# Performance work log

Hardware: AMD Instinct MI355X
Metric: run time of the kernel (lower is better)

The kernel has to match this reference:

```python
import jax, jax.numpy as jnp
import numpy as np

B, L, D, H = 2, 2048, 1024, 16
HD = D // H
SCALE = 1.0 / (HD ** 0.5)


def setup_inputs() -> dict:
    key = jax.random.key(0)
    ks = jax.random.split(key, 8)
    s = 0.02  # keep pre-softmax logits in a sane range
    return {
        "x": jax.random.normal(ks[0], (B, L, D), dtype=jnp.float32),
        "attn_biases": jax.random.normal(ks[1], (B, H, L, L), dtype=jnp.float32) * 0.1,
        "attn_mask": jnp.zeros((B, 1, L, L), dtype=jnp.float32),
        "Wq": jax.random.normal(ks[2], (D, D), dtype=jnp.float32) * s,
        "bq": jnp.zeros((D,), dtype=jnp.float32),
        "Wk": jax.random.normal(ks[3], (D, D), dtype=jnp.float32) * s,
        "bk": jnp.zeros((D,), dtype=jnp.float32),
        "Wv": jax.random.normal(ks[4], (D, D), dtype=jnp.float32) * s,
        "bv": jnp.zeros((D,), dtype=jnp.float32),
        "Wo": jax.random.normal(ks[5], (D, D), dtype=jnp.float32) * s,
        "bo": jnp.zeros((D,), dtype=jnp.float32),
    }


def reference(x, attn_biases, attn_mask, Wq, bq, Wk, bk, Wv, bv, Wo, bo):
    b, l, d = x.shape
    # torch nn.Linear: y = x @ W.T + b
    q = (x @ Wq.T + bq).reshape(b, l, H, HD)
    k = (x @ Wk.T + bk).reshape(b, l, H, HD)
    v = (x @ Wv.T + bv).reshape(b, l, H, HD)
    # scores: (B, H, Lq, Lk)
    scores = SCALE * jnp.einsum("bqhd,bkhd->bhqk", q, k)
    scores = scores + attn_biases + attn_mask
    probs = jax.nn.softmax(scores, axis=-1)
    out = jnp.einsum("bhqk,bkhd->bqhd", probs, v).reshape(b, l, d)
    return out @ Wo.T + bo
```

## Files before the change

### kernel.cpp

```cpp
#include <hip/hip_runtime.h>
#include <stdint.h>

#define SCALE_ 0.125f

typedef unsigned short u16;
typedef __attribute__((ext_vector_type(8))) __bf16 bf16x8;
typedef __attribute__((ext_vector_type(4))) float f32x4;
typedef __attribute__((ext_vector_type(4))) unsigned int u32x4;

__device__ __forceinline__ void gload16(const void* g, void* l) {
  __builtin_amdgcn_global_load_lds(
      (const __attribute__((address_space(1))) unsigned int*)g,
      (__attribute__((address_space(3))) unsigned int*)l, 16, 0, 0);
}

__device__ __forceinline__ u16 f2bf(float f) {
  union { float f; unsigned int u; } v; v.f = f;
  return (u16)((v.u + 0x7FFFu + ((v.u >> 16) & 1u)) >> 16);
}

__device__ __forceinline__ bf16x8 ld_bf8(const u16* p) {
  return *reinterpret_cast<const bf16x8*>(p);
}

__global__ __launch_bounds__(256) void cvt_kernel(
    const float* __restrict__ x, const float* __restrict__ wq,
    const float* __restrict__ wk, const float* __restrict__ wv,
    const float* __restrict__ wo, u16* __restrict__ ws) {
  long e0 = ((long)blockIdx.x * 256 + threadIdx.x) * 8;
  const float* src; u16* dst; long off;
  if (e0 < 4194304L) {
    src = x; dst = ws; off = e0;
  } else {
    long tt = e0 - 4194304L;
    int w = (int)(tt >> 20);
    off = tt & 1048575L;
    src = (w == 0) ? wq : (w == 1) ? wk : (w == 2) ? wv : wo;
    dst = ws + 4194304L + (long)w * 1048576L;
  }
  float4 f0 = *(const float4*)(src + off);
  float4 f1 = *(const float4*)(src + off + 4);
  union { u16 u[8]; u32x4 v; } r;
  r.u[0] = f2bf(f0.x); r.u[1] = f2bf(f0.y); r.u[2] = f2bf(f0.z); r.u[3] = f2bf(f0.w);
  r.u[4] = f2bf(f1.x); r.u[5] = f2bf(f1.y); r.u[6] = f2bf(f1.z); r.u[7] = f2bf(f1.w);
  *reinterpret_cast<u32x4*>(dst + off) = r.v;
}

__global__ __launch_bounds__(256) void gemm_bt(
    const u16* __restrict__ A,
    const u16* __restrict__ W0, const u16* __restrict__ W1, const u16* __restrict__ W2,
    const float* __restrict__ b0, const float* __restrict__ b1, const float* __restrict__ b2,
    void* __restrict__ d0, void* __restrict__ d1, void* __restrict__ d2,
    int mode_base) {
  __shared__ u16 lsA[128 * 32];
  __shared__ u16 lsB[128 * 32];

  const int z = blockIdx.z;
  const int mode = mode_base + z;
  const u16* W = (z == 0) ? W0 : (z == 1) ? W1 : W2;
  const float* bias = (z == 0) ? b0 : (z == 1) ? b1 : b2;
  void* dst = (z == 0) ? d0 : (z == 1) ? d1 : d2;
  const float scale = (mode == 0) ? SCALE_ : 1.0f;

  const int t = threadIdx.x;
  const int bm = blockIdx.y, bn = blockIdx.x;
  const int lane = t & 63, lr = lane & 15, lg = lane >> 4;
  const int wid = t >> 6, wr = wid >> 1, wc = wid & 1;

  f32x4 zero = {0.f, 0.f, 0.f, 0.f};
  f32x4 acc[4][4];
#pragma unroll
  for (int i = 0; i < 4; ++i)
#pragma unroll
    for (int j = 0; j < 4; ++j) acc[i][j] = zero;

  const u16* gA = A + (size_t)(bm * 128) * 1024;
  const u16* gB = W + (size_t)(bn * 128) * 1024;
  const int srow = t >> 2, scol = (t & 3) * 8;

  for (int kt = 0; kt < 32; ++kt) {
    const int k0 = kt * 32;
    __syncthreads();
    gload16(gA + (size_t)srow * 1024 + k0 + scol,        &lsA[t * 8]);
    gload16(gA + (size_t)(srow + 64) * 1024 + k0 + scol, &lsA[2048 + t * 8]);
    gload16(gB + (size_t)srow * 1024 + k0 + scol,        &lsB[t * 8]);
    gload16(gB + (size_t)(srow + 64) * 1024 + k0 + scol, &lsB[2048 + t * 8]);
    __syncthreads();

    bf16x8 af[4], bf[4];
#pragma unroll
    for (int mi = 0; mi < 4; ++mi)
      af[mi] = ld_bf8(&lsA[(wr * 64 + mi * 16 + lr) * 32 + lg * 8]);
#pragma unroll
    for (int ni = 0; ni < 4; ++ni)
      bf[ni] = ld_bf8(&lsB[(wc * 64 + ni * 16 + lr) * 32 + lg * 8]);
#pragma unroll
    for (int mi = 0; mi < 4; ++mi)
#pragma unroll
      for (int ni = 0; ni < 4; ++ni)
        acc[mi][ni] = __builtin_amdgcn_mfma_f32_16x16x32_bf16(af[mi], bf[ni], acc[mi][ni], 0, 0, 0);
  }

#pragma unroll
  for (int ni = 0; ni < 4; ++ni) {
    const int gcol = bn * 128 + wc * 64 + ni * 16 + lr;
    const float bv = bias[gcol];
#pragma unroll
    for (int mi = 0; mi < 4; ++mi) {
      const int growb = bm * 128 + wr * 64 + mi * 16 + lg * 4;
#pragma unroll
      for (int j = 0; j < 4; ++j) {
        const int grow = growb + j;
        const float val = (acc[mi][ni][j] + bv) * scale;
        if (mode == 3) {
          ((float*)dst)[(size_t)grow * 1024 + gcol] = val;
        } else {
          const int b = grow >> 11, l = grow & 2047, h = gcol >> 6, hd = gcol & 63;
          size_t idx;
          if (mode == 2) idx = (((size_t)(b * 16 + h)) * 64 + hd) * 2048 + l;
          else           idx = (((size_t)(b * 16 + h)) * 2048 + l) * 64 + hd;
          ((u16*)dst)[idx] = f2bf(val);
        }
      }
    }
  }
}

__global__ __launch_bounds__(256) void gemm_out64(
    const u16* __restrict__ A, const u16* __restrict__ W,
    const float* __restrict__ bias, float* __restrict__ out) {
  __shared__ u16 lsA[64 * 32];
  __shared__ u16 lsB[128 * 32];

  const int t = threadIdx.x;
  const int bm = blockIdx.y, bn = blockIdx.x;
  const int lane = t & 63, lr = lane & 15, lg = lane >> 4;
  const int wid = t >> 6;

  f32x4 zero = {0.f, 0.f, 0.f, 0.f};
  f32x4 acc[4][2];
#pragma unroll
  for (int i = 0; i < 4; ++i) { acc[i][0] = zero; acc[i][1] = zero; }

  const u16* gA = A + (size_t)(bm * 64) * 1024;
  const u16* gB = W + (size_t)(bn * 128) * 1024;
  const int srow = t >> 2, scol = (t & 3) * 8;

  for (int kt = 0; kt < 32; ++kt) {
    const int k0 = kt * 32;
    __syncthreads();
    gload16(gA + (size_t)srow * 1024 + k0 + scol,        &lsA[t * 8]);
    gload16(gB + (size_t)srow * 1024 + k0 + scol,        &lsB[t * 8]);
    gload16(gB + (size_t)(srow + 64) * 1024 + k0 + scol, &lsB[2048 + t * 8]);
    __syncthreads();

    bf16x8 af[4], bf[2];
#pragma unroll
    for (int mi = 0; mi < 4; ++mi)
      af[mi] = ld_bf8(&lsA[(mi * 16 + lr) * 32 + lg * 8]);
#pragma unroll
    for (int ni = 0; ni < 2; ++ni)
      bf[ni] = ld_bf8(&lsB[(wid * 32 + ni * 16 + lr) * 32 + lg * 8]);
#pragma unroll
    for (int mi = 0; mi < 4; ++mi)
#pragma unroll
      for (int ni = 0; ni < 2; ++ni)
        acc[mi][ni] = __builtin_amdgcn_mfma_f32_16x16x32_bf16(af[mi], bf[ni], acc[mi][ni], 0, 0, 0);
  }

#pragma unroll
  for (int ni = 0; ni < 2; ++ni) {
    const int gcol = bn * 128 + wid * 32 + ni * 16 + lr;
    const float bv = bias[gcol];
#pragma unroll
    for (int mi = 0; mi < 4; ++mi) {
      const int growb = bm * 64 + mi * 16 + lg * 4;
#pragma unroll
      for (int j = 0; j < 4; ++j)
        out[(size_t)(growb + j) * 1024 + gcol] = acc[mi][ni][j] + bv;
    }
  }
}

__global__ __launch_bounds__(256, 4) void attn_kernel(
    const u16* __restrict__ Q, const u16* __restrict__ Kb_, const u16* __restrict__ Vtb,
    const float* __restrict__ bias, const float* __restrict__ mask,
    u16* __restrict__ attn) {
  __shared__ u16 lsK[64 * 64];
  __shared__ u16 lsV[64 * 64];
  __shared__ u16 lsP[4][16 * 80];

  const int t = threadIdx.x, wid = t >> 6, lane = t & 63, lr = lane & 15, lg = lane >> 4;
  const int q0 = blockIdx.x * 64;
  const int h = blockIdx.y, b = blockIdx.z;
  const int bh = b * 16 + h;

  const u16* qb = Q + ((size_t)bh * 2048 + q0 + wid * 16) * 64;
  const u16* kb = Kb_ + (size_t)bh * 2048 * 64;
  const u16* vb = Vtb + (size_t)bh * 64 * 2048;
  const float* biasr = bias + (size_t)bh * 2048 * 2048;
  const float* maskr = mask + (size_t)b * 2048 * 2048;

  bf16x8 qf[2];
  qf[0] = ld_bf8(qb + (size_t)lr * 64 + lg * 8);
  qf[1] = ld_bf8(qb + (size_t)lr * 64 + 32 + lg * 8);

  float m[4] = {-1e30f, -1e30f, -1e30f, -1e30f};
  float lsum[4] = {0.f, 0.f, 0.f, 0.f};
  f32x4 zero = {0.f, 0.f, 0.f, 0.f};
  f32x4 o[4];
#pragma unroll
  for (int i = 0; i < 4; ++i) o[i] = zero;

  const int srow = t >> 3;
  const int swz = ((t & 7) ^ (srow & 7)) * 8;
  const int rsw = (lr & 7) * 8;
  const int qrow0 = q0 + wid * 16 + lg * 4;

  for (int kt = 0; kt < 32; ++kt) {
    const int k0 = kt * 64;

    float bb[4][4];
#pragma unroll
    for (int j = 0; j < 4; ++j) {
      const float* br = biasr + (size_t)(qrow0 + j) * 2048 + k0 + lr;
      const float* mr = maskr + (size_t)(qrow0 + j) * 2048 + k0 + lr;
#pragma unroll
      for (int n = 0; n < 4; ++n) bb[j][n] = br[n * 16] + mr[n * 16];
    }

    __syncthreads();
    gload16(kb + (size_t)(k0 + srow) * 64 + swz,        &lsK[t * 8]);
    gload16(kb + (size_t)(k0 + srow + 32) * 64 + swz,   &lsK[2048 + t * 8]);
    gload16(vb + (size_t)srow * 2048 + k0 + swz,        &lsV[t * 8]);
    gload16(vb + (size_t)(srow + 32) * 2048 + k0 + swz, &lsV[2048 + t * 8]);
    __syncthreads();

    f32x4 s[4];
#pragma unroll
    for (int n = 0; n < 4; ++n) s[n] = zero;
#pragma unroll
    for (int ks = 0; ks < 2; ++ks)
#pragma unroll
      for (int n = 0; n < 4; ++n) {
        bf16x8 kf = ld_bf8(&lsK[((n * 16 + lr) * 64 + ks * 32 + lg * 8) ^ rsw]);
        s[n] = __builtin_amdgcn_mfma_f32_16x16x32_bf16(qf[ks], kf, s[n], 0, 0, 0);
      }

#pragma unroll
    for (int j = 0; j < 4; ++j)
#pragma unroll
      for (int n = 0; n < 4; ++n) s[n][j] += bb[j][n];

    float corr[4];
#pragma unroll
    for (int i = 0; i < 4; ++i) {
      float mx = fmaxf(fmaxf(s[0][i], s[1][i]), fmaxf(s[2][i], s[3][i]));
      mx = fmaxf(mx, __shfl_xor(mx, 1));
      mx = fmaxf(mx, __shfl_xor(mx, 2));
      mx = fmaxf(mx, __shfl_xor(mx, 4));
      mx = fmaxf(mx, __shfl_xor(mx, 8));
      const float mnew = fmaxf(m[i], mx);
      const float c = __expf(m[i] - mnew);
      m[i] = mnew;
      float rs = 0.f;
#pragma unroll
      for (int n = 0; n < 4; ++n) {
        float p = __expf(s[n][i] - mnew);
        s[n][i] = p;
        rs += p;
      }
      rs += __shfl_xor(rs, 1); rs += __shfl_xor(rs, 2);
      rs += __shfl_xor(rs, 4); rs += __shfl_xor(rs, 8);
      lsum[i] = lsum[i] * c + rs;
      corr[i] = c;
    }
#pragma unroll
    for (int dt = 0; dt < 4; ++dt)
#pragma unroll
      for (int i = 0; i < 4; ++i) o[dt][i] *= corr[i];

#pragma unroll
    for (int n = 0; n < 4; ++n)
#pragma unroll
      for (int i = 0; i < 4; ++i)
        lsP[wid][(lg * 4 + i) * 80 + n * 16 + lr] = f2bf(s[n][i]);
    asm volatile("s_waitcnt lgkmcnt(0)" ::: "memory");
    __builtin_amdgcn_sched_barrier(0);

#pragma unroll
    for (int ks = 0; ks < 2; ++ks) {
      bf16x8 pa = ld_bf8(&lsP[wid][lr * 80 + ks * 32 + lg * 8]);
#pragma unroll
      for (int dt = 0; dt < 4; ++dt) {
        bf16x8 vf = ld_bf8(&lsV[((dt * 16 + lr) * 64 + ks * 32 + lg * 8) ^ rsw]);
        o[dt] = __builtin_amdgcn_mfma_f32_16x16x32_bf16(pa, vf, o[dt], 0, 0, 0);
      }
    }
  }

  float inv[4];
#pragma unroll
  for (int i = 0; i < 4; ++i) inv[i] = 1.0f / lsum[i];
#pragma unroll
  for (int dt = 0; dt < 4; ++dt) {
    const int dcol = h * 64 + dt * 16 + lr;
#pragma unroll
    for (int i = 0; i < 4; ++i)
      attn[((size_t)b * 2048 + qrow0 + i) * 1024 + dcol] = f2bf(o[dt][i] * inv[i]);
  }
}

extern "C" void kernel_launch(void* const* d_in, const int* in_sizes, int n_in,
                              void* d_out, int out_size, void* d_ws, size_t ws_size,
                              hipStream_t stream) {
  const float* x    = (const float*)d_in[0];
  const float* bias = (const float*)d_in[1];
  const float* mask = (const float*)d_in[2];
  const float* Wq   = (const float*)d_in[3];
  const float* bq   = (const float*)d_in[4];
  const float* Wk   = (const float*)d_in[5];
  const float* bk   = (const float*)d_in[6];
  const float* Wv   = (const float*)d_in[7];
  const float* bv   = (const float*)d_in[8];
  const float* Wo   = (const float*)d_in[9];
  const float* bo   = (const float*)d_in[10];
  float* out = (float*)d_out;

  u16* ws   = (u16*)d_ws;
  u16* xb   = ws;
  u16* wqb  = ws + 4194304L;
  u16* wkb  = wqb + 1048576L;
  u16* wvb  = wkb + 1048576L;
  u16* wob  = wvb + 1048576L;
  u16* Qb   = wob + 1048576L;
  u16* Kb   = Qb + 4194304L;
  u16* Vtb  = Kb + 4194304L;
  u16* attnb = Vtb + 4194304L;

  cvt_kernel<<<4096, 256, 0, stream>>>(x, Wq, Wk, Wv, Wo, ws);

  dim3 gqkv(8, 32, 3);
  gemm_bt<<<gqkv, 256, 0, stream>>>(xb, wqb, wkb, wvb, bq, bk, bv,
                                    (void*)Qb, (void*)Kb, (void*)Vtb, 0);

  attn_kernel<<<dim3(32, 16, 2), 256, 0, stream>>>(Qb, Kb, Vtb, bias, mask, attnb);

  gemm_out64<<<dim3(8, 64), 256, 0, stream>>>(attnb, wob, bo, out);
}
```

Before: 250.5 us.

## Prefetch next K/V tile and bias through registers to overlap with compute

Replaces the synchronous global_load_lds staging of K/V tiles with register prefetch: the next tile's K/V are loaded into registers at the start of each iteration and written to LDS after the PV MFMAs. Bias and mask loads for the next tile are also issued early, so their latency hides behind the softmax and matmul work. The trade-off is higher register pressure and an extra register-to-LDS write step, and the last iteration does one redundant reload.

```diff
diff --git a/kernel.cpp b/kernel.cpp
--- a/kernel.cpp
+++ b/kernel.cpp
@@ -212,29 +212,42 @@
 #pragma unroll
   for (int i = 0; i < 4; ++i) o[i] = zero;
 
-  const int srow = t >> 3;
-  const int swz = ((t & 7) ^ (srow & 7)) * 8;
+  const int srow = t >> 3, schunk = t & 7;
+  const int swc = (schunk ^ (srow & 7)) * 8;
+  const int gco = schunk * 8;
   const int rsw = (lr & 7) * 8;
   const int qrow0 = q0 + wid * 16 + lg * 4;
 
+  u16* wK0 = &lsK[srow * 64 + swc];
+  u16* wK1 = &lsK[(srow + 32) * 64 + swc];
+  u16* wV0 = &lsV[srow * 64 + swc];
+  u16* wV1 = &lsV[(srow + 32) * 64 + swc];
+
+  u32x4 rk0 = *(const u32x4*)(kb + (size_t)srow * 64 + gco);
+  u32x4 rk1 = *(const u32x4*)(kb + (size_t)(srow + 32) * 64 + gco);
+  u32x4 rv0 = *(const u32x4*)(vb + (size_t)srow * 2048 + gco);
+  u32x4 rv1 = *(const u32x4*)(vb + (size_t)(srow + 32) * 2048 + gco);
+  *(u32x4*)wK0 = rk0; *(u32x4*)wK1 = rk1;
+  *(u32x4*)wV0 = rv0; *(u32x4*)wV1 = rv1;
+  __syncthreads();
+
+  float bb[4][4];
+#pragma unroll
+  for (int j = 0; j < 4; ++j) {
+    const float* br = biasr + (size_t)(qrow0 + j) * 2048 + lr;
+    const float* mr = maskr + (size_t)(qrow0 + j) * 2048 + lr;
+#pragma unroll
+    for (int n = 0; n < 4; ++n) bb[j][n] = br[n * 16] + mr[n * 16];
+  }
+
   for (int kt = 0; kt < 32; ++kt) {
-    const int k0 = kt * 64;
-
-    float bb[4][4];
-#pragma unroll
-    for (int j = 0; j < 4; ++j) {
-      const float* br = biasr + (size_t)(qrow0 + j) * 2048 + k0 + lr;
-      const float* mr = maskr + (size_t)(qrow0 + j) * 2048 + k0 + lr;
-#pragma unroll
-      for (int n = 0; n < 4; ++n) bb[j][n] = br[n * 16] + mr[n * 16];
-    }
-
-    __syncthreads();
-    gload16(kb + (size_t)(k0 + srow) * 64 + swz,        &lsK[t * 8]);
-    gload16(kb + (size_t)(k0 + srow + 32) * 64 + swz,   &lsK[2048 + t * 8]);
-    gload16(vb + (size_t)srow * 2048 + k0 + swz,        &lsV[t * 8]);
-    gload16(vb + (size_t)(srow + 32) * 2048 + k0 + swz, &lsV[2048 + t * 8]);
-    __syncthreads();
+    const int ktn = (kt < 31) ? kt + 1 : 31;
+    const int k0n = ktn * 64;
+
+    rk0 = *(const u32x4*)(kb + (size_t)(k0n + srow) * 64 + gco);
+    rk1 = *(const u32x4*)(kb + (size_t)(k0n + srow + 32) * 64 + gco);
+    rv0 = *(const u32x4*)(vb + (size_t)srow * 2048 + k0n + gco);
+    rv1 = *(const u32x4*)(vb + (size_t)(srow + 32) * 2048 + k0n + gco);
 
     f32x4 s[4];
 #pragma unroll
@@ -252,7 +265,14 @@
 #pragma unroll
       for (int n = 0; n < 4; ++n) s[n][j] += bb[j][n];
 
-    float corr[4];
+#pragma unroll
+    for (int j = 0; j < 4; ++j) {
+      const float* br = biasr + (size_t)(qrow0 + j) * 2048 + k0n + lr;
+      const float* mr = maskr + (size_t)(qrow0 + j) * 2048 + k0n + lr;
+#pragma unroll
+      for (int n = 0; n < 4; ++n) bb[j][n] = br[n * 16] + mr[n * 16];
+    }
+
 #pragma unroll
     for (int i = 0; i < 4; ++i) {
       float mx = fmaxf(fmaxf(s[0][i], s[1][i]), fmaxf(s[2][i], s[3][i]));
@@ -273,12 +293,8 @@
       rs += __shfl_xor(rs, 1); rs += __shfl_xor(rs, 2);
       rs += __shfl_xor(rs, 4); rs += __shfl_xor(rs, 8);
       lsum[i] = lsum[i] * c + rs;
-      corr[i] = c;
-    }
-#pragma unroll
-    for (int dt = 0; dt < 4; ++dt)
-#pragma unroll
-      for (int i = 0; i < 4; ++i) o[dt][i] *= corr[i];
+      o[0][i] *= c; o[1][i] *= c; o[2][i] *= c; o[3][i] *= c;
+    }
 
 #pragma unroll
     for (int n = 0; n < 4; ++n)
@@ -297,6 +313,11 @@
         o[dt] = __builtin_amdgcn_mfma_f32_16x16x32_bf16(pa, vf, o[dt], 0, 0, 0);
       }
     }
+
+    __syncthreads();
+    *(u32x4*)wK0 = rk0; *(u32x4*)wK1 = rk1;
+    *(u32x4*)wV0 = rv0; *(u32x4*)wV1 = rv1;
+    __syncthreads();
   }
 
   float inv[4];
```

Measured after the change: 354.0 us. 1.41x slower.
